# Kernel optimization log

Measured on AMD Instinct MI355X. Metric: run time of the kernel, lower is better.

The kernel has to match this reference:

```python
import jax, jax.numpy as jnp
import numpy as np
from jax import lax

B, H, W, C_IN, C_OUT = 32, 56, 56, 256, 256
KH, KW = 3, 3

def setup_inputs() -> dict:
    key = jax.random.key(0)
    k_in, k_kern, k_bias = jax.random.split(key, 3)
    inputs = jax.random.normal(k_in, (B, H, W, C_IN), dtype=jnp.float32)
    # lecun_normal (flax default_kernel_init): std = 1/sqrt(fan_in)
    fan_in = KH * KW * C_IN
    kernel = jax.random.normal(k_kern, (KH, KW, C_IN, C_OUT), dtype=jnp.float32) / jnp.sqrt(fan_in).astype(jnp.float32)
    bias = jnp.zeros((C_OUT,), dtype=jnp.float32)
    return {"inputs": inputs, "kernel": kernel, "bias": bias}

def reference(inputs, kernel, bias):
    # QuantConv forward with config noise == 0.0: plain NHWC/HWIO conv + bias.
    y = lax.conv_general_dilated(
        inputs, kernel,
        window_strides=(1, 1),
        padding='SAME',
        lhs_dilation=(1, 1),
        rhs_dilation=(1, 1),
        dimension_numbers=('NHWC', 'HWIO', 'NHWC'),
        feature_group_count=1,
    )
    return y + bias
```

## Files before the change

kernel.cpp:

```cpp
#include <hip/hip_runtime.h>
#include <hip/hip_bf16.h>
#include <stdint.h>


#define IMG_B 32
#define IMG_H 56
#define IMG_W 56
#define CIN   256
#define COUT  256
#define KDIM  2304
#define M_TOT 100352
#define HW    (IMG_H * IMG_W)
#define PW    58
#define PHW   (PW * PW)
#define BK    64
#define ITERS (KDIM / BK)
#define TILE_E (128 * BK)
#define PAD_BLOCKS 13456
#define WT_BLOCKS  (KDIM * COUT / 256)

typedef __bf16 bf16_t;
typedef bf16_t bf16x8 __attribute__((ext_vector_type(8)));
typedef float  f32x4  __attribute__((ext_vector_type(4)));
typedef float  f32x16 __attribute__((ext_vector_type(16)));

typedef const __attribute__((address_space(1))) void GV;
typedef __attribute__((address_space(3))) void LV;

__device__ __forceinline__ void async16(const bf16_t* g, bf16_t* l) {
    __builtin_amdgcn_global_load_lds((GV*)g, (LV*)l, 16, 0, 0);
}

__global__ void prep_fused(const float* __restrict__ in, const float* __restrict__ kern,
                           bf16_t* __restrict__ pimg, bf16_t* __restrict__ wt) {
    if (blockIdx.x < PAD_BLOCKS) {
        const size_t e = ((size_t)blockIdx.x * 256 + threadIdx.x) * 8;
        const int pix = (int)(e >> 8);
        const int c0  = (int)(e & 255);
        const int b   = pix / PHW;
        const int r   = pix - b * PHW;
        const int py  = r / PW;
        const int px  = r - py * PW;
        bf16x8 v = {};
        if (py >= 1 && py <= IMG_H && px >= 1 && px <= IMG_W) {
            const f32x4* s = (const f32x4*)(in +
                ((((size_t)b * IMG_H + (py - 1)) * IMG_W + (px - 1)) << 8) + c0);
            f32x4 a = s[0], bq = s[1];
            #pragma unroll
            for (int k = 0; k < 4; ++k) v[k] = (bf16_t)a[k];
            #pragma unroll
            for (int k = 0; k < 4; ++k) v[4 + k] = (bf16_t)bq[k];
        }
        *(bf16x8*)(pimg + e) = v;
    } else {
        const int idx = (blockIdx.x - PAD_BLOCKS) * 256 + threadIdx.x;
        const int co  = idx / KDIM;
        const int k   = idx - co * KDIM;
        wt[idx] = (bf16_t)kern[k * COUT + co];
    }
}

__global__ void prep_weights(const float* __restrict__ kern, bf16_t* __restrict__ wt) {
    int idx = blockIdx.x * 256 + threadIdx.x;
    int co  = idx / KDIM;
    int k   = idx - co * KDIM;
    wt[idx] = (bf16_t)kern[k * COUT + co];
}


#define STAGE(t1, cb) do { \
    const int tap_  = (t1) >> 2; \
    const int kh_   = tap_ / 3; \
    const int kw_   = tap_ - kh_ * 3; \
    const int koff_ = ((kh_ * PW + kw_) << 8) + (((t1) & 3) << 6); \
    const int woff_ = (t1) * BK; \
    _Pragma("unroll") \
    for (int i_ = 0; i_ < 4; ++i_) { \
        async16(asrc[i_] + koff_, alds[i_] + (cb) * TILE_E); \
        async16(bsrc[i_] + woff_, blds[i_] + (cb) * TILE_E); \
    } \
} while (0)

#define STEP(t, cur) do { \
    if ((t) + 1 < ITERS) asm volatile("s_waitcnt vmcnt(8)" ::: "memory"); \
    else                 asm volatile("s_waitcnt vmcnt(0)" ::: "memory"); \
    __builtin_amdgcn_s_barrier(); \
    __builtin_amdgcn_sched_barrier(0); \
    bf16x8 af[2][4], bfr[2][4]; \
    _Pragma("unroll") \
    for (int kk = 0; kk < 4; ++kk) { \
        const int slot_ = ((kk * 2 + lh) ^ rx) * 8; \
        af[0][kk]  = *(const bf16x8*)(&Al[cur][(wm * 64 + ln) * BK + slot_]); \
        af[1][kk]  = *(const bf16x8*)(&Al[cur][(wm * 64 + 32 + ln) * BK + slot_]); \
        bfr[0][kk] = *(const bf16x8*)(&Bl[cur][(wn * 64 + ln) * BK + slot_]); \
        bfr[1][kk] = *(const bf16x8*)(&Bl[cur][(wn * 64 + 32 + ln) * BK + slot_]); \
    } \
    asm volatile("s_waitcnt lgkmcnt(0)" ::: "memory"); \
    __builtin_amdgcn_s_barrier(); \
    __builtin_amdgcn_sched_barrier(0); \
    if ((t) + 2 < ITERS) STAGE((t) + 2, cur); \
    __builtin_amdgcn_s_setprio(1); \
    _Pragma("unroll") \
    for (int kk = 0; kk < 4; ++kk) { \
        acc[0][0] = __builtin_amdgcn_mfma_f32_32x32x16_bf16(af[0][kk], bfr[0][kk], acc[0][0], 0, 0, 0); \
        acc[0][1] = __builtin_amdgcn_mfma_f32_32x32x16_bf16(af[0][kk], bfr[1][kk], acc[0][1], 0, 0, 0); \
        acc[1][0] = __builtin_amdgcn_mfma_f32_32x32x16_bf16(af[1][kk], bfr[0][kk], acc[1][0], 0, 0, 0); \
        acc[1][1] = __builtin_amdgcn_mfma_f32_32x32x16_bf16(af[1][kk], bfr[1][kk], acc[1][1], 0, 0, 0); \
    } \
    __builtin_amdgcn_s_setprio(0); \
} while (0)

__global__ __launch_bounds__(256)
void conv_mfma_p(const bf16_t* __restrict__ P, const bf16_t* __restrict__ wt,
                 const float* __restrict__ bias, float* __restrict__ out)
{
    __shared__ bf16_t Al[2][TILE_E];
    __shared__ bf16_t Bl[2][TILE_E];

    const int tid  = threadIdx.x;
    const int wave = tid >> 6;
    const int lane = tid & 63;

    const int bid   = blockIdx.x;
    const int tile  = (bid & 7) * 196 + (bid >> 3);
    const int ntile = tile & 1;
    const int mtile = tile >> 1;

    const int rl = lane >> 3;
    const int sl = lane & 7;
    const int u  = sl ^ rl;

    const bf16_t* asrc[4];
    const bf16_t* bsrc[4];
    bf16_t* alds[4];
    bf16_t* blds[4];
    #pragma unroll
    for (int i = 0; i < 4; ++i) {
        const int row = wave * 32 + i * 8 + rl;
        const int m   = mtile * 128 + row;
        const int bb  = m / HW;
        const int rem = m - bb * HW;
        const int yy  = rem / IMG_W;
        const int xx  = rem - yy * IMG_W;
        asrc[i] = P + (((size_t)bb * PHW + yy * PW + xx) << 8) + u * 8;
        const int co = ntile * 128 + row;
        bsrc[i] = wt + (size_t)co * KDIM + u * 8;
        alds[i] = &Al[0][(wave * 32 + i * 8) * BK];
        blds[i] = &Bl[0][(wave * 32 + i * 8) * BK];
    }

    const int wm = wave & 1;
    const int wn = wave >> 1;
    const int ln = lane & 31;
    const int lh = lane >> 5;
    const int rx = ln & 7;

    f32x16 acc[2][2] = {};

    STAGE(0, 0);
    STAGE(1, 1);

    #pragma unroll 1
    for (int it2 = 0; it2 < ITERS / 2; ++it2) {
        const int t0 = it2 * 2;
        STEP(t0,     0);
        STEP(t0 + 1, 1);
    }

    const int mbase  = mtile * 128 + wm * 64;
    const int cobase = ntile * 128 + wn * 64;
    float bv[2];
    bv[0] = bias[cobase + ln];
    bv[1] = bias[cobase + 32 + ln];

    #pragma unroll
    for (int g = 0; g < 2; ++g) {
        #pragma unroll
        for (int reg = 0; reg < 16; ++reg) {
            const int mm = mbase + g * 32 + (reg & 3) + 8 * (reg >> 2) + 4 * lh;
            float* op = out + (size_t)mm * COUT + cobase + ln;
            op[0]  = acc[g][0][reg] + bv[0];
            op[32] = acc[g][1][reg] + bv[1];
        }
    }
}

#define ASTR 40
#define BSTR 40
__global__ __launch_bounds__(256)
void conv_mfma(const float* __restrict__ in, const bf16_t* __restrict__ wt,
               const float* __restrict__ bias, float* __restrict__ out)
{
    __shared__ bf16_t Alf[128 * ASTR];
    __shared__ bf16_t Blf[128 * BSTR];

    const int tid   = threadIdx.x;
    const int ntile = blockIdx.x & 1;
    const int mtile = blockIdx.x >> 1;

    const int arow = tid >> 1;
    const int aseg = tid & 1;
    const int m    = mtile * 128 + arow;
    const int bb   = m / HW;
    const int rem  = m - bb * HW;
    const int yy   = rem / IMG_W;
    const int xx   = rem - yy * IMG_W;

    const bf16_t* wt_row = wt + (size_t)(ntile * 128 + arow) * KDIM + aseg * 16;

    const int wave = tid >> 6;
    const int lane = tid & 63;
    const int wm   = wave & 1;
    const int wn   = wave >> 1;
    const int lrow = lane & 15;
    const int q    = lane >> 4;

    f32x4 acc[4][4] = {};

    #pragma unroll 1
    for (int it = 0; it < 72; ++it) {
        const int tap = it >> 3;
        const int kh  = tap / 3;
        const int kw  = tap - kh * 3;
        const int ci0 = (it & 7) << 5;

        const int iy = yy + kh - 1;
        const int ix = xx + kw - 1;
        const bool valid = ((unsigned)iy < IMG_H) && ((unsigned)ix < IMG_W);

        f32x4 va[4] = {};
        if (valid) {
            const f32x4* src = (const f32x4*)(in +
                ((((size_t)bb * IMG_H + iy) * IMG_W + ix) * CIN + ci0 + aseg * 16));
            va[0] = src[0]; va[1] = src[1]; va[2] = src[2]; va[3] = src[3];
        }
        const uint4 wb0 = *(const uint4*)(wt_row + it * 32);
        const uint4 wb1 = *(const uint4*)(wt_row + it * 32 + 8);

        __syncthreads();

        bf16x8 pa0, pa1;
        #pragma unroll
        for (int e = 0; e < 8; ++e) pa0[e] = (bf16_t)va[e >> 2][e & 3];
        #pragma unroll
        for (int e = 0; e < 8; ++e) pa1[e] = (bf16_t)va[2 + (e >> 2)][e & 3];
        *(bf16x8*)(&Alf[arow * ASTR + aseg * 16])     = pa0;
        *(bf16x8*)(&Alf[arow * ASTR + aseg * 16 + 8]) = pa1;
        *(uint4*)(&Blf[arow * BSTR + aseg * 16])      = wb0;
        *(uint4*)(&Blf[arow * BSTR + aseg * 16 + 8])  = wb1;

        __syncthreads();

        bf16x8 af[4], bf[4];
        #pragma unroll
        for (int i = 0; i < 4; ++i)
            af[i] = *(const bf16x8*)(&Alf[(wm * 64 + i * 16 + lrow) * ASTR + q * 8]);
        #pragma unroll
        for (int j = 0; j < 4; ++j)
            bf[j] = *(const bf16x8*)(&Blf[(wn * 64 + j * 16 + lrow) * BSTR + q * 8]);

        #pragma unroll
        for (int i = 0; i < 4; ++i)
            #pragma unroll
            for (int j = 0; j < 4; ++j)
                acc[i][j] = __builtin_amdgcn_mfma_f32_16x16x32_bf16(af[i], bf[j], acc[i][j], 0, 0, 0);
    }

    const int co_base = ntile * 128 + wn * 64;
    float bv[4];
    #pragma unroll
    for (int j = 0; j < 4; ++j) bv[j] = bias[co_base + j * 16 + lrow];

    const int mrow_base = mtile * 128 + wm * 64;
    #pragma unroll
    for (int i = 0; i < 4; ++i) {
        #pragma unroll
        for (int rr = 0; rr < 4; ++rr) {
            const int mm = mrow_base + i * 16 + q * 4 + rr;
            float* op = out + (size_t)mm * COUT + co_base;
            #pragma unroll
            for (int j = 0; j < 4; ++j)
                op[j * 16 + lrow] = acc[i][j][rr] + bv[j];
        }
    }
}

extern "C" void kernel_launch(void* const* d_in, const int* in_sizes, int n_in,
                              void* d_out, int out_size, void* d_ws, size_t ws_size,
                              hipStream_t stream) {
    const float* inputs = (const float*)d_in[0];
    const float* kernel = (const float*)d_in[1];
    const float* bias   = (const float*)d_in[2];
    float*       outp   = (float*)d_out;

    const size_t p_elems = (size_t)IMG_B * PHW * CIN;
    const size_t p_bytes = p_elems * sizeof(bf16_t);
    const size_t w_bytes = (size_t)KDIM * COUT * sizeof(bf16_t);

    if (ws_size >= p_bytes + w_bytes) {
        bf16_t* pimg = (bf16_t*)d_ws;
        bf16_t* wt   = (bf16_t*)((char*)d_ws + p_bytes);
        prep_fused<<<PAD_BLOCKS + WT_BLOCKS, 256, 0, stream>>>(inputs, kernel, pimg, wt);
        conv_mfma_p<<<(M_TOT / 128) * 2, 256, 0, stream>>>(pimg, wt, bias, outp);
    } else {
        bf16_t* wt = (bf16_t*)d_ws;
        prep_weights<<<WT_BLOCKS, 256, 0, stream>>>(kernel, wt);
        conv_mfma<<<(M_TOT / 128) * 2, 256, 0, stream>>>(inputs, wt, bias, outp);
    }
}
```

Measured before the change: 321.4 us.

## Load weight fragments directly from global into registers, bypassing LDS

The weight prep now writes bf16 weights pre-arranged in MFMA fragment order, so each lane can load its B operand straight from global memory into registers. That removes the B tile from LDS and its LDS reads. The A pipeline drops from two stages ahead to one, uses a single __syncthreads per step, and occupancy is hinted with launch_bounds(256,2). In exchange, every wave issues redundant global/L2 reads of weights, the A prefetch depth is shallower, and register pressure rises because of double-buffered B fragments.

```diff
diff --git a/kernel.cpp b/kernel.cpp
--- a/kernel.cpp
+++ b/kernel.cpp
@@ -32,7 +32,7 @@
 }
 
 __global__ void prep_fused(const float* __restrict__ in, const float* __restrict__ kern,
-                           bf16_t* __restrict__ pimg, bf16_t* __restrict__ wt) {
+                           bf16_t* __restrict__ pimg, bf16_t* __restrict__ wt2) {
     if (blockIdx.x < PAD_BLOCKS) {
         const size_t e = ((size_t)blockIdx.x * 256 + threadIdx.x) * 8;
         const int pix = (int)(e >> 8);
@@ -54,9 +54,14 @@
         *(bf16x8*)(pimg + e) = v;
     } else {
         const int idx = (blockIdx.x - PAD_BLOCKS) * 256 + threadIdx.x;
-        const int co  = idx / KDIM;
-        const int k   = idx - co * KDIM;
-        wt[idx] = (bf16_t)kern[k * COUT + co];
+        const int e  = idx & 7;
+        const int l  = (idx >> 3) & 63;
+        const int kk = (idx >> 9) & 3;
+        const int n  = (idx >> 11) & 7;
+        const int t  = idx >> 14;
+        const int co = n * 32 + (l & 31);
+        const int k  = t * 64 + kk * 16 + (l >> 5) * 8 + e;
+        wt2[idx] = (bf16_t)kern[k * COUT + co];
     }
 }
 
@@ -68,54 +73,52 @@
 }
 
 
-#define STAGE(t1, cb) do { \
+#define STAGE_A(t1, cb) do { \
     const int tap_  = (t1) >> 2; \
     const int kh_   = tap_ / 3; \
     const int kw_   = tap_ - kh_ * 3; \
     const int koff_ = ((kh_ * PW + kw_) << 8) + (((t1) & 3) << 6); \
-    const int woff_ = (t1) * BK; \
     _Pragma("unroll") \
-    for (int i_ = 0; i_ < 4; ++i_) { \
+    for (int i_ = 0; i_ < 4; ++i_) \
         async16(asrc[i_] + koff_, alds[i_] + (cb) * TILE_E); \
-        async16(bsrc[i_] + woff_, blds[i_] + (cb) * TILE_E); \
-    } \
 } while (0)
 
-#define STEP(t, cur) do { \
-    if ((t) + 1 < ITERS) asm volatile("s_waitcnt vmcnt(8)" ::: "memory"); \
-    else                 asm volatile("s_waitcnt vmcnt(0)" ::: "memory"); \
-    __builtin_amdgcn_s_barrier(); \
-    __builtin_amdgcn_sched_barrier(0); \
-    bf16x8 af[2][4], bfr[2][4]; \
+#define LOADB(t1, dst) do { \
+    const size_t tb_ = (size_t)(t1) * 16384; \
+    _Pragma("unroll") \
+    for (int h_ = 0; h_ < 2; ++h_) \
+        _Pragma("unroll") \
+        for (int kk_ = 0; kk_ < 4; ++kk_) \
+            dst[h_][kk_] = *(const bf16x8*)(pB[h_] + tb_ + kk_ * 512); \
+} while (0)
+
+#define STEP(t, cur, bcur, bnxt) do { \
+    __syncthreads(); \
+    if ((t) + 1 < ITERS) STAGE_A((t) + 1, (cur) ^ 1); \
+    bf16x8 af[2][4]; \
     _Pragma("unroll") \
     for (int kk = 0; kk < 4; ++kk) { \
         const int slot_ = ((kk * 2 + lh) ^ rx) * 8; \
-        af[0][kk]  = *(const bf16x8*)(&Al[cur][(wm * 64 + ln) * BK + slot_]); \
-        af[1][kk]  = *(const bf16x8*)(&Al[cur][(wm * 64 + 32 + ln) * BK + slot_]); \
-        bfr[0][kk] = *(const bf16x8*)(&Bl[cur][(wn * 64 + ln) * BK + slot_]); \
-        bfr[1][kk] = *(const bf16x8*)(&Bl[cur][(wn * 64 + 32 + ln) * BK + slot_]); \
+        af[0][kk] = *(const bf16x8*)(&Al[cur][(wm * 64 + ln) * BK + slot_]); \
+        af[1][kk] = *(const bf16x8*)(&Al[cur][(wm * 64 + 32 + ln) * BK + slot_]); \
     } \
-    asm volatile("s_waitcnt lgkmcnt(0)" ::: "memory"); \
-    __builtin_amdgcn_s_barrier(); \
-    __builtin_amdgcn_sched_barrier(0); \
-    if ((t) + 2 < ITERS) STAGE((t) + 2, cur); \
+    if ((t) + 1 < ITERS) LOADB((t) + 1, bnxt); \
     __builtin_amdgcn_s_setprio(1); \
     _Pragma("unroll") \
     for (int kk = 0; kk < 4; ++kk) { \
-        acc[0][0] = __builtin_amdgcn_mfma_f32_32x32x16_bf16(af[0][kk], bfr[0][kk], acc[0][0], 0, 0, 0); \
-        acc[0][1] = __builtin_amdgcn_mfma_f32_32x32x16_bf16(af[0][kk], bfr[1][kk], acc[0][1], 0, 0, 0); \
-        acc[1][0] = __builtin_amdgcn_mfma_f32_32x32x16_bf16(af[1][kk], bfr[0][kk], acc[1][0], 0, 0, 0); \
-        acc[1][1] = __builtin_amdgcn_mfma_f32_32x32x16_bf16(af[1][kk], bfr[1][kk], acc[1][1], 0, 0, 0); \
+        acc[0][0] = __builtin_amdgcn_mfma_f32_32x32x16_bf16(af[0][kk], bcur[0][kk], acc[0][0], 0, 0, 0); \
+        acc[0][1] = __builtin_amdgcn_mfma_f32_32x32x16_bf16(af[0][kk], bcur[1][kk], acc[0][1], 0, 0, 0); \
+        acc[1][0] = __builtin_amdgcn_mfma_f32_32x32x16_bf16(af[1][kk], bcur[0][kk], acc[1][0], 0, 0, 0); \
+        acc[1][1] = __builtin_amdgcn_mfma_f32_32x32x16_bf16(af[1][kk], bcur[1][kk], acc[1][1], 0, 0, 0); \
     } \
     __builtin_amdgcn_s_setprio(0); \
 } while (0)
 
-__global__ __launch_bounds__(256)
-void conv_mfma_p(const bf16_t* __restrict__ P, const bf16_t* __restrict__ wt,
+__global__ __launch_bounds__(256, 2)
+void conv_mfma_p(const bf16_t* __restrict__ P, const bf16_t* __restrict__ wt2,
                  const float* __restrict__ bias, float* __restrict__ out)
 {
     __shared__ bf16_t Al[2][TILE_E];
-    __shared__ bf16_t Bl[2][TILE_E];
 
     const int tid  = threadIdx.x;
     const int wave = tid >> 6;
@@ -131,9 +134,7 @@
     const int u  = sl ^ rl;
 
     const bf16_t* asrc[4];
-    const bf16_t* bsrc[4];
     bf16_t* alds[4];
-    bf16_t* blds[4];
     #pragma unroll
     for (int i = 0; i < 4; ++i) {
         const int row = wave * 32 + i * 8 + rl;
@@ -143,10 +144,7 @@
         const int yy  = rem / IMG_W;
         const int xx  = rem - yy * IMG_W;
         asrc[i] = P + (((size_t)bb * PHW + yy * PW + xx) << 8) + u * 8;
-        const int co = ntile * 128 + row;
-        bsrc[i] = wt + (size_t)co * KDIM + u * 8;
         alds[i] = &Al[0][(wave * 32 + i * 8) * BK];
-        blds[i] = &Bl[0][(wave * 32 + i * 8) * BK];
     }
 
     const int wm = wave & 1;
@@ -155,16 +153,21 @@
     const int lh = lane >> 5;
     const int rx = ln & 7;
 
+    const bf16_t* pB[2];
+    #pragma unroll
+    for (int h = 0; h < 2; ++h)
+        pB[h] = wt2 + (size_t)(ntile * 4 + 2 * wn + h) * 2048 + lane * 8;
+
     f32x16 acc[2][2] = {};
-
-    STAGE(0, 0);
-    STAGE(1, 1);
+    bf16x8 bf0[2][4], bf1[2][4];
+
+    STAGE_A(0, 0);
+    LOADB(0, bf0);
 
     #pragma unroll 1
-    for (int it2 = 0; it2 < ITERS / 2; ++it2) {
-        const int t0 = it2 * 2;
-        STEP(t0,     0);
-        STEP(t0 + 1, 1);
+    for (int t2 = 0; t2 < ITERS / 2; ++t2) {
+        STEP(t2 * 2,     0, bf0, bf1);
+        STEP(t2 * 2 + 1, 1, bf1, bf0);
     }
 
     const int mbase  = mtile * 128 + wm * 64;
@@ -299,9 +302,9 @@
 
     if (ws_size >= p_bytes + w_bytes) {
         bf16_t* pimg = (bf16_t*)d_ws;
-        bf16_t* wt   = (bf16_t*)((char*)d_ws + p_bytes);
-        prep_fused<<<PAD_BLOCKS + WT_BLOCKS, 256, 0, stream>>>(inputs, kernel, pimg, wt);
-        conv_mfma_p<<<(M_TOT / 128) * 2, 256, 0, stream>>>(pimg, wt, bias, outp);
+        bf16_t* wt2  = (bf16_t*)((char*)d_ws + p_bytes);
+        prep_fused<<<PAD_BLOCKS + WT_BLOCKS, 256, 0, stream>>>(inputs, kernel, pimg, wt2);
+        conv_mfma_p<<<(M_TOT / 128) * 2, 256, 0, stream>>>(pimg, wt2, bias, outp);
     } else {
         bf16_t* wt = (bf16_t*)d_ws;
         prep_weights<<<WT_BLOCKS, 256, 0, stream>>>(kernel, wt);
```

Result: slower. 331.4 us (+3.1%).
